# Optimization experiments

Hardware: AMD Instinct MI355X
Metric: run time of the kernel (lower is better)

The kernel has to match this reference:

```python
import jax, jax.numpy as jnp
import numpy as np

B, N, E, F, FE, H = 4, 1024, 65536, 96, 32, 12
DH = F // H
EPS = 1e-3  # keras LayerNormalization default epsilon


def layer_norm(x, g, b):
    m = jnp.mean(x, axis=-1, keepdims=True)
    v = jnp.var(x, axis=-1, keepdims=True)
    return (x - m) / jnp.sqrt(v + EPS) * g + b


def setup_inputs() -> dict:
    key = jax.random.key(0)
    ks = jax.random.split(key, 14)
    s = lambda d: 1.0 / np.sqrt(d)
    return {
        "nodes": jax.random.normal(ks[0], (B, N, F), jnp.float32),
        "edge_features": jax.random.normal(ks[1], (B, E, FE), jnp.float32),
        "distance": jax.random.uniform(ks[2], (B, E, 1), jnp.float32),
        "edges": jax.random.randint(ks[3], (B, E, 2), 0, N, jnp.int32),
        # message MLP: Dense(2F+FE -> F) + GELU + LayerNorm
        "Wm": jax.random.normal(ks[4], (2 * F + FE, F), jnp.float32) * s(2 * F + FE),
        "bm": jnp.zeros((F,), jnp.float32),
        "g1": jnp.ones((F,), jnp.float32),
        "b1": jnp.zeros((F,), jnp.float32),
        # gated multi-head self-attention over concat([nodes, aggregated]) (2F -> F)
        "Wq": jax.random.normal(ks[5], (2 * F, F), jnp.float32) * s(2 * F),
        "bq": jnp.zeros((F,), jnp.float32),
        "Wk": jax.random.normal(ks[6], (2 * F, F), jnp.float32) * s(2 * F),
        "bk": jnp.zeros((F,), jnp.float32),
        "Wv": jax.random.normal(ks[7], (2 * F, F), jnp.float32) * s(2 * F),
        "bv": jnp.zeros((F,), jnp.float32),
        "Wg": jax.random.normal(ks[8], (2 * F, F), jnp.float32) * s(2 * F),
        "bg": jnp.zeros((F,), jnp.float32),
        "Wo": jax.random.normal(ks[9], (F, F), jnp.float32) * s(F),
        "bo": jnp.zeros((F,), jnp.float32),
        "g2": jnp.ones((F,), jnp.float32),
        "b2": jnp.zeros((F,), jnp.float32),
        # learnable gaussian edge-weight params
        "sigma": jnp.full((1,), 0.005, jnp.float32),
        "beta": jnp.full((1,), 4.0, jnp.float32),
    }


def reference(nodes, edge_features, distance, edges, Wm, bm, g1, b1,
              Wq, bq, Wk, bk, Wv, bv, Wg, bg, Wo, bo, g2, b2, sigma, beta):
    # --- message: gather endpoint node features per edge ---
    gathered = jax.vmap(lambda n, e: n[e])(nodes, edges)              # [B,E,2,F]
    msg_in = jnp.concatenate([gathered.reshape(B, E, 2 * F), edge_features], axis=-1)
    messages = layer_norm(jax.nn.gelu(msg_in @ Wm + bm, approximate=False), g1, b1)  # [B,E,F]
    # --- learnable gaussian edge weighting ---
    edge_weights = jnp.exp(-((distance ** 2 / (2.0 * sigma ** 2)) ** beta))           # [B,E,1]
    weighted_messages = messages * edge_weights
    # --- scatter: per-graph segment-sum into receiver nodes (edge[:,1]) ---
    aggregated = jax.vmap(lambda m, seg: jax.ops.segment_sum(m, seg, num_segments=N))(
        weighted_messages, edges[..., 1])                             # [B,N,F]
    # --- update: gated multi-head self-attention on concat([nodes, aggregated]) ---
    x = jnp.concatenate([nodes, aggregated], axis=-1)                 # [B,N,2F]
    heads = lambda t: t.reshape(B, N, H, DH).transpose(0, 2, 1, 3)    # [B,H,N,DH]
    q, k, v = heads(x @ Wq + bq), heads(x @ Wk + bk), heads(x @ Wv + bv)
    gate = heads(jax.nn.sigmoid(x @ Wg + bg))
    attn = jax.nn.softmax(jnp.einsum("bhqd,bhkd->bhqk", q, k) / jnp.sqrt(jnp.float32(DH)), axis=-1)
    out = (jnp.einsum("bhqk,bhkd->bhqd", attn, v) * gate).transpose(0, 2, 1, 3).reshape(B, N, F)
    out = out @ Wo + bo
    updated_nodes = layer_norm(jax.nn.gelu(out, approximate=False), g2, b2)
    return (updated_nodes, weighted_messages, distance, edges)
```

## Files before the change

kernel.cpp:

```cpp
#include <hip/hip_runtime.h>
#include <math.h>

#define Bn 4
#define Nn 1024
#define En 65536
#define Fn 96
#define FEn 32
#define Hn 12

#define OUT_UPD  0
#define OUT_WM   393216LL
#define OUT_DIST 25559040LL
#define OUT_EDGE 25821184LL

#define WS_AGG  0
#define WS_Q    393216
#define WS_K    786432
#define WS_V    1179648
#define WS_G    1572864
#define WS_AO   1966080
#define WS_LIST 2359296
#define WS_LW   2424832
#define WS_CNT  2490368

#define MSG_BLOCKS 832

typedef __attribute__((ext_vector_type(8))) short bf16x8;
typedef __attribute__((ext_vector_type(4))) float f32x4;

__device__ __forceinline__ float gelu_exact(float x) {
    return 0.5f * x * (1.0f + erff(x * 0.70710678118654752f));
}

__device__ __forceinline__ unsigned cvtpk_bf16(float lo, float hi) {
    unsigned r;
    asm("v_cvt_pk_bf16_f32 %0, %1, %2" : "=v"(r) : "v"(lo), "v"(hi));
    return r;
}

__device__ __forceinline__ void zero_wm_chunk(int c, const float* __restrict__ dist,
                                              const float* __restrict__ sigma,
                                              const float* __restrict__ beta,
                                              float* __restrict__ out_wm,
                                              int tid, int nthr, int* s_act) {
    if (tid < 256) {
        int ge = c * 256 + tid;
        float d = dist[ge];
        float sg = sigma[0], bt = beta[0];
        float t = d * d / (2.0f * sg * sg);
        s_act[tid] = (powf(t, bt) < 90.0f) ? 1 : 0;
    }
    __syncthreads();
    const float4 z = make_float4(0.f, 0.f, 0.f, 0.f);
    float4* wm4 = (float4*)out_wm + (size_t)c * 6144;
    for (int p = tid; p < 6144; p += nthr) {
        if (!s_act[p / 24]) wm4[p] = z;
    }
}

__global__ void zero_kernel(float* __restrict__ agg, int* __restrict__ gcnt) {
    int i = blockIdx.x * 256 + threadIdx.x;
    const float4 z = make_float4(0.f, 0.f, 0.f, 0.f);
    float4* p = (float4*)agg;
    p[i] = z;
    p[i + 49152] = z;
    if (i == 0) gcnt[0] = 0;
}

__global__ __launch_bounds__(1024) void scan_kernel(
        const float* __restrict__ dist, const int* __restrict__ edges,
        const float* __restrict__ sigma, const float* __restrict__ beta,
        float* __restrict__ out_dist, float* __restrict__ out_edges,
        int* __restrict__ glist, float* __restrict__ gw,
        int* __restrict__ gcnt) {
    __shared__ int wcnt[16], wbase[16], blkbase;
    int tid = threadIdx.x;
    int lane = tid & 63, wv = tid >> 6;
    int ge = blockIdx.x * 1024 + tid;
    float d = dist[ge];
    out_dist[ge] = d;
    int e0 = edges[2 * ge], e1 = edges[2 * ge + 1];
    *(float2*)&out_edges[2 * ge] = make_float2((float)e0, (float)e1);
    float sg = sigma[0], bt = beta[0];
    float t  = d * d / (2.0f * sg * sg);
    float tp = powf(t, bt);
    bool active = (tp < 90.0f);
    float w = active ? expf(-tp) : 0.0f;

    unsigned long long mask = __ballot(active);
    int lp = __popcll(mask & ((1ull << lane) - 1ull));
    if (lane == 0) wcnt[wv] = __popcll(mask);
    __syncthreads();
    if (tid == 0) {
        int a = 0;
        #pragma unroll
        for (int i = 0; i < 16; ++i) { wbase[i] = a; a += wcnt[i]; }
        blkbase = a ? atomicAdd(gcnt, a) : 0;
    }
    __syncthreads();
    if (active) {
        int pos = blkbase + wbase[wv] + lp;
        if (pos < 65536) { glist[pos] = ge; gw[pos] = w; }
    }
}

__global__ __launch_bounds__(256) void msg_kernel(
        const int* __restrict__ glist, const float* __restrict__ gw,
        const int* __restrict__ gcnt, const int* __restrict__ edges,
        const float* __restrict__ nodes, const float* __restrict__ ef,
        const float* __restrict__ Wm, const float* __restrict__ bm,
        const float* __restrict__ g1, const float* __restrict__ b1,
        float* __restrict__ out_wm, float* __restrict__ agg) {
    __shared__ float sin_s[4][4][232];
    int tid = threadIdx.x;
    int lane = tid & 63, wv = tid >> 6;
    int count = gcnt[0];
    if (count > 65536) count = 65536;
    if ((int)blockIdx.x * 16 >= count) return;
    int c2 = 64 + (lane & 31);
    int wid = blockIdx.x * 4 + wv;

    for (int base = wid * 4; base < count; base += MSG_BLOCKS * 16) {
        int   gei[4];
        float wgt[4];
        bool  val[4];
        #pragma unroll
        for (int e = 0; e < 4; ++e) {
            int ai = base + e;
            val[e] = (ai < count);
            int as = val[e] ? ai : base;
            gei[e] = glist[as];
            wgt[e] = val[e] ? gw[ai] : 0.0f;
        }
        #pragma unroll
        for (int e = 0; e < 4; ++e) {
            int g = gei[e];
            int b = g >> 16;
            int e0 = edges[2 * g], e1 = edges[2 * g + 1];
            const float* n0 = nodes + ((size_t)b * Nn + e0) * 96;
            const float* n1 = nodes + ((size_t)b * Nn + e1) * 96;
            const float* ep = ef + (size_t)g * 32;
            #pragma unroll
            for (int ii = 0; ii < 4; ++ii) {
                int i = ii * 64 + lane;
                if (i < 224) {
                    float v = (i < 96) ? n0[i] : (i < 192) ? n1[i - 96] : ep[i - 192];
                    sin_s[wv][e][i] = v;
                }
            }
        }
        float acc[4][2];
        #pragma unroll
        for (int e = 0; e < 4; ++e) { acc[e][0] = bm[lane]; acc[e][1] = bm[c2]; }
        #pragma unroll 8
        for (int i = 0; i < 224; ++i) {
            float w1 = Wm[i * 96 + lane];
            float w2 = Wm[i * 96 + c2];
            #pragma unroll
            for (int e = 0; e < 4; ++e) {
                float a = sin_s[wv][e][i];
                acc[e][0] = fmaf(a, w1, acc[e][0]);
                acc[e][1] = fmaf(a, w2, acc[e][1]);
            }
        }
        #pragma unroll
        for (int e = 0; e < 4; ++e) {
            if (!val[e]) continue;
            float y1 = gelu_exact(acc[e][0]);
            float y2 = gelu_exact(acc[e][1]);
            float c2v = (lane < 32) ? y2 : 0.0f;
            float sum  = y1 + c2v;
            float sum2 = y1 * y1 + c2v * c2v;
            #pragma unroll
            for (int off = 1; off < 64; off <<= 1) {
                sum  += __shfl_xor(sum, off);
                sum2 += __shfl_xor(sum2, off);
            }
            float mean = sum * (1.0f / 96.0f);
            float var  = sum2 * (1.0f / 96.0f) - mean * mean;
            float rs   = rsqrtf(var + 1e-3f);
            int g = gei[e];
            int b = g >> 16;
            int e1 = edges[2 * g + 1];
            float* aggp = agg + ((size_t)b * Nn + e1) * 96;
            float* wmp  = out_wm + (size_t)g * 96;
            float o1 = ((y1 - mean) * rs * g1[lane] + b1[lane]) * wgt[e];
            wmp[lane] = o1;
            atomicAdd(&aggp[lane], o1);
            if (lane < 32) {
                float o2 = ((y2 - mean) * rs * g1[c2] + b1[c2]) * wgt[e];
                wmp[c2] = o2;
                atomicAdd(&aggp[c2], o2);
            }
        }
    }
}

__global__ __launch_bounds__(256, 1) void proj_kernel(
        const float* __restrict__ nodes, const float* __restrict__ agg,
        const float* __restrict__ Wq, const float* __restrict__ bq,
        const float* __restrict__ Wk, const float* __restrict__ bk,
        const float* __restrict__ Wv, const float* __restrict__ bv,
        const float* __restrict__ Wg, const float* __restrict__ bg,
        float* __restrict__ qo, float* __restrict__ ko,
        float* __restrict__ vo, float* __restrict__ go,
        const float* __restrict__ dist, const float* __restrict__ sigma,
        const float* __restrict__ beta, float* __restrict__ out_wm) {
    __shared__ float xs[192][64];
    __shared__ float Ws[192 * 96];
    __shared__ int s_act[256];
    int tid = threadIdx.x;
    int m = blockIdx.y;
    zero_wm_chunk(768 + m * 64 + blockIdx.x, dist, sigma, beta, out_wm, tid, 256, s_act);

    const float* W    = (m == 0) ? Wq : (m == 1) ? Wk : (m == 2) ? Wv : Wg;
    const float* bias = (m == 0) ? bq : (m == 1) ? bk : (m == 2) ? bv : bg;
    float* outp       = (m == 0) ? qo : (m == 1) ? ko : (m == 2) ? vo : go;
    int row0 = blockIdx.x * 64;
    int b = row0 >> 10, n0 = row0 & 1023;

    {
        float4* Ws4 = (float4*)Ws;
        const float4* Wg4 = (const float4*)W;
        for (int i = tid; i < 4608; i += 256) Ws4[i] = Wg4[i];
    }
    for (int i = tid; i < 3072; i += 256) {
        int r = i & 63, k4 = i >> 6;
        size_t row = (size_t)row0 + r;
        float4 v = (k4 < 24) ? *(const float4*)&nodes[row * 96 + k4 * 4]
                             : *(const float4*)&agg[row * 96 + (k4 - 24) * 4];
        int k = k4 * 4;
        xs[k][r] = v.x; xs[k + 1][r] = v.y; xs[k + 2][r] = v.z; xs[k + 3][r] = v.w;
    }
    __syncthreads();

    int lane = tid & 63;
    int wcol = __builtin_amdgcn_readfirstlane((tid >> 6) * 24);
    float acc[24];
    #pragma unroll
    for (int c = 0; c < 24; ++c) acc[c] = bias[wcol + c];
    for (int k = 0; k < 192; ++k) {
        float a = xs[k][lane];
        const float* wr = &Ws[k * 96 + wcol];
        #pragma unroll
        for (int c = 0; c < 24; ++c)
            acc[c] = fmaf(a, wr[c], acc[c]);
    }
    if (m == 3) {
        #pragma unroll
        for (int c = 0; c < 24; ++c) acc[c] = 1.0f / (1.0f + expf(-acc[c]));
    }
    float4* out4 = (float4*)outp;
    int h0 = wcol >> 3;
    #pragma unroll
    for (int hh = 0; hh < 3; ++hh) {
        size_t base = (((size_t)b * Hn + (h0 + hh)) * Nn + (n0 + lane)) * 2;
        out4[base]     = make_float4(acc[hh*8+0], acc[hh*8+1], acc[hh*8+2], acc[hh*8+3]);
        out4[base + 1] = make_float4(acc[hh*8+4], acc[hh*8+5], acc[hh*8+6], acc[hh*8+7]);
    }
}

__global__ __launch_bounds__(256, 4) void attn_kernel(
        const float* __restrict__ qp, const float* __restrict__ kp,
        const float* __restrict__ vp, const float* __restrict__ gp,
        float* __restrict__ ao,
        const float* __restrict__ dist, const float* __restrict__ sigma,
        const float* __restrict__ beta, float* __restrict__ out_wm) {
    __shared__ __align__(16) unsigned short K_s[1024][8];
    __shared__ __align__(16) unsigned short Vt_s[9][1032];
    __shared__ __align__(16) unsigned short P_s[4][16][32];
    __shared__ int s_act[256];
    int tid = threadIdx.x;
    zero_wm_chunk(blockIdx.y * 16 + blockIdx.x, dist, sigma, beta, out_wm, tid, 256, s_act);

    int bh = blockIdx.y;
    int lane = tid & 63, wv = tid >> 6;
    size_t hb = (size_t)bh * (Nn * 8);
    const float* kc = kp + hb;
    const float* vc = vp + hb;

    {
        const float2* k2 = (const float2*)kc;
        unsigned* kw = (unsigned*)&K_s[0][0];
        for (int i = tid; i < 4096; i += 256) {
            float2 v = k2[i];
            kw[i] = cvtpk_bf16(v.x, v.y);
        }
    }
    {
        const float4* v4 = (const float4*)vc;
        for (int i = tid; i < 1024; i += 256) {
            int kp2 = i >> 1, dq = i & 1;
            float4 a = v4[kp2 * 4 + dq];
            float4 b = v4[kp2 * 4 + 2 + dq];
            int d0 = dq * 4;
            ((unsigned*)&Vt_s[d0 + 0][0])[kp2] = cvtpk_bf16(a.x, b.x);
            ((unsigned*)&Vt_s[d0 + 1][0])[kp2] = cvtpk_bf16(a.y, b.y);
            ((unsigned*)&Vt_s[d0 + 2][0])[kp2] = cvtpk_bf16(a.z, b.z);
            ((unsigned*)&Vt_s[d0 + 3][0])[kp2] = cvtpk_bf16(a.w, b.w);
        }
        unsigned* ow = (unsigned*)&Vt_s[8][0];
        for (int i = tid; i < 516; i += 256) ow[i] = 0x3F803F80u;
    }
    const float scale = 0.35355339059327376f;
    int qbase = blockIdx.x * 64 + wv * 16;
    bf16x8 aq = {0, 0, 0, 0, 0, 0, 0, 0};
    if (lane < 16) {
        const float* qr = qp + hb + (size_t)(qbase + lane) * 8;
        float4 qa = *(const float4*)qr;
        float4 qb2 = *(const float4*)(qr + 4);
        union { unsigned u[4]; bf16x8 v; } U;
        U.u[0] = cvtpk_bf16(qa.x * scale, qa.y * scale);
        U.u[1] = cvtpk_bf16(qa.z * scale, qa.w * scale);
        U.u[2] = cvtpk_bf16(qb2.x * scale, qb2.y * scale);
        U.u[3] = cvtpk_bf16(qb2.z * scale, qb2.w * scale);
        aq = U.v;
    }
    __syncthreads();

    const bf16x8 zero8 = {0, 0, 0, 0, 0, 0, 0, 0};
    const f32x4 zero4 = {0.f, 0.f, 0.f, 0.f};
    f32x4 o = zero4;
    int n16 = lane & 15, grp = lane >> 4;
    for (int c = 0; c < 32; ++c) {
        bf16x8 bk0 = zero8, bk1 = zero8;
        if (lane < 16) {
            bk0 = *(const bf16x8*)&K_s[c * 32 + lane][0];
            bk1 = *(const bf16x8*)&K_s[c * 32 + 16 + lane][0];
        }
        f32x4 s0 = __builtin_amdgcn_mfma_f32_16x16x32_bf16(aq, bk0, zero4, 0, 0, 0);
        f32x4 s1 = __builtin_amdgcn_mfma_f32_16x16x32_bf16(aq, bk1, zero4, 0, 0, 0);
        #pragma unroll
        for (int r = 0; r < 4; ++r) {
            unsigned pk = cvtpk_bf16(__expf(s0[r]), __expf(s1[r]));
            int row = grp * 4 + r;
            P_s[wv][row][n16]      = (unsigned short)pk;
            P_s[wv][row][16 + n16] = (unsigned short)(pk >> 16);
        }
        bf16x8 pa = *(const bf16x8*)&P_s[wv][n16][grp * 8];
        bf16x8 bv = zero8;
        if (n16 <= 8) bv = *(const bf16x8*)&Vt_s[n16][c * 32 + grp * 8];
        o = __builtin_amdgcn_mfma_f32_16x16x32_bf16(pa, bv, o, 0, 0, 0);
    }

    #pragma unroll
    for (int r = 0; r < 4; ++r) {
        float L = __shfl(o[r], (lane & 48) | 8);
        if (n16 < 8) {
            int q = qbase + grp * 4 + r;
            size_t off = hb + (size_t)q * 8 + n16;
            ao[off] = o[r] / L * gp[off];
        }
    }
}

__global__ __launch_bounds__(256) void out_kernel(
        const float* __restrict__ ao, const float* __restrict__ Wo,
        const float* __restrict__ bo, const float* __restrict__ g2,
        const float* __restrict__ b2, float* __restrict__ out0) {
    __shared__ float as_[96][64];
    __shared__ float Ws[96 * 96];
    __shared__ float2 red_s[4][64];
    int tid = threadIdx.x;
    int row0 = blockIdx.x * 64;
    int b = row0 >> 10, n0 = row0 & 1023;
    {
        float4* W4 = (float4*)Ws;
        const float4* Wg4 = (const float4*)Wo;
        for (int i = tid; i < 2304; i += 256) W4[i] = Wg4[i];
    }
    const float2* ao2 = (const float2*)ao;
    for (int i = tid; i < 3072; i += 256) {
        int n = i & 63, hd = i >> 6;
        int h = hd >> 2, dp = hd & 3;
        float2 v = ao2[(((size_t)b * Hn + h) * Nn + (n0 + n)) * 4 + dp];
        as_[h * 8 + dp * 2][n]     = v.x;
        as_[h * 8 + dp * 2 + 1][n] = v.y;
    }
    __syncthreads();
    int lane = tid & 63, w = tid >> 6;
    int wcol = __builtin_amdgcn_readfirstlane(w * 24);
    float acc[24];
    #pragma unroll
    for (int c = 0; c < 24; ++c) acc[c] = bo[wcol + c];
    for (int k = 0; k < 96; ++k) {
        float a = as_[k][lane];
        const float* wr = &Ws[k * 96 + wcol];
        #pragma unroll
        for (int c = 0; c < 24; ++c)
            acc[c] = fmaf(a, wr[c], acc[c]);
    }
    float y[24];
    float sum = 0.0f, sum2 = 0.0f;
    #pragma unroll
    for (int c = 0; c < 24; ++c) {
        float g = gelu_exact(acc[c]);
        y[c] = g; sum += g; sum2 += g * g;
    }
    red_s[w][lane] = make_float2(sum, sum2);
    __syncthreads();
    float S = 0.0f, S2 = 0.0f;
    #pragma unroll
    for (int i = 0; i < 4; ++i) { float2 p = red_s[i][lane]; S += p.x; S2 += p.y; }
    float mean = S * (1.0f / 96.0f);
    float var  = S2 * (1.0f / 96.0f) - mean * mean;
    float rs   = rsqrtf(var + 1e-3f);
    size_t row = (size_t)row0 + lane;
    #pragma unroll
    for (int c = 0; c < 24; ++c)
        y[c] = (y[c] - mean) * rs * g2[wcol + c] + b2[wcol + c];
    float4* o4 = (float4*)&out0[row * 96 + wcol];
    #pragma unroll
    for (int q = 0; q < 6; ++q)
        o4[q] = make_float4(y[q*4], y[q*4+1], y[q*4+2], y[q*4+3]);
}

extern "C" void kernel_launch(void* const* d_in, const int* in_sizes, int n_in,
                              void* d_out, int out_size, void* d_ws, size_t ws_size,
                              hipStream_t stream) {
    const float* nodes = (const float*)d_in[0];
    const float* ef    = (const float*)d_in[1];
    const float* dist  = (const float*)d_in[2];
    const int*   edges = (const int*)d_in[3];
    const float* Wm = (const float*)d_in[4];
    const float* bm = (const float*)d_in[5];
    const float* g1 = (const float*)d_in[6];
    const float* b1 = (const float*)d_in[7];
    const float* Wq = (const float*)d_in[8];
    const float* bq = (const float*)d_in[9];
    const float* Wk = (const float*)d_in[10];
    const float* bk = (const float*)d_in[11];
    const float* Wv = (const float*)d_in[12];
    const float* bv = (const float*)d_in[13];
    const float* Wg = (const float*)d_in[14];
    const float* bg = (const float*)d_in[15];
    const float* Wo = (const float*)d_in[16];
    const float* bo = (const float*)d_in[17];
    const float* g2 = (const float*)d_in[18];
    const float* b2 = (const float*)d_in[19];
    const float* sigma = (const float*)d_in[20];
    const float* beta  = (const float*)d_in[21];

    float* out = (float*)d_out;
    float* ws  = (float*)d_ws;

    float* agg  = ws + WS_AGG;
    float* qb   = ws + WS_Q;
    float* kb   = ws + WS_K;
    float* vb   = ws + WS_V;
    float* gwb  = ws + WS_G;
    float* aob  = ws + WS_AO;
    int*   glist = (int*)(ws + WS_LIST);
    float* glw   = ws + WS_LW;
    int*   gcnt  = (int*)(ws + WS_CNT);

    zero_kernel<<<192, 256, 0, stream>>>(agg, gcnt);

    scan_kernel<<<Bn * En / 1024, 1024, 0, stream>>>(
        dist, edges, sigma, beta, out + OUT_DIST, out + OUT_EDGE, glist, glw, gcnt);

    msg_kernel<<<MSG_BLOCKS, 256, 0, stream>>>(
        glist, glw, gcnt, edges, nodes, ef, Wm, bm, g1, b1, out + OUT_WM, agg);

    dim3 gp_(64, 4);
    proj_kernel<<<gp_, 256, 0, stream>>>(
        nodes, agg, Wq, bq, Wk, bk, Wv, bv, Wg, bg, qb, kb, vb, gwb,
        dist, sigma, beta, out + OUT_WM);

    dim3 ga(16, Bn * Hn);
    attn_kernel<<<ga, 256, 0, stream>>>(qb, kb, vb, gwb, aob,
                                        dist, sigma, beta, out + OUT_WM);

    out_kernel<<<Bn * Nn / 64, 256, 0, stream>>>(aob, Wo, bo, g2, b2, out + OUT_UPD);
}
```

Measured before the change: 110.2 us.

## Fuse edge scan and message computation into one per-block kernel

Combines the global active-edge compaction and the message MLP into a single kernel where each 256-edge block compacts its active edges in shared memory and processes them locally. This drops the global atomic counter, the global list buffers, a separate zero kernel and a launch. The zeroing of inactive weighted-message rows moves out of the projection and attention kernels into the fused kernel. The trade-off is possible load imbalance, since work per block now depends on how many active edges it holds, and the agg buffer is cleared with a memset.

After: 103.1 us. -6.5%, faster.

```diff
diff --git a/kernel.cpp b/kernel.cpp
--- a/kernel.cpp
+++ b/kernel.cpp
@@ -19,11 +19,6 @@
 #define WS_V    1179648
 #define WS_G    1572864
 #define WS_AO   1966080
-#define WS_LIST 2359296
-#define WS_LW   2424832
-#define WS_CNT  2490368
-
-#define MSG_BLOCKS 832
 
 typedef __attribute__((ext_vector_type(8))) short bf16x8;
 typedef __attribute__((ext_vector_type(4))) float f32x4;
@@ -38,99 +33,72 @@
     return r;
 }
 
-__device__ __forceinline__ void zero_wm_chunk(int c, const float* __restrict__ dist,
-                                              const float* __restrict__ sigma,
-                                              const float* __restrict__ beta,
-                                              float* __restrict__ out_wm,
-                                              int tid, int nthr, int* s_act) {
-    if (tid < 256) {
-        int ge = c * 256 + tid;
-        float d = dist[ge];
-        float sg = sigma[0], bt = beta[0];
-        float t = d * d / (2.0f * sg * sg);
-        s_act[tid] = (powf(t, bt) < 90.0f) ? 1 : 0;
-    }
-    __syncthreads();
-    const float4 z = make_float4(0.f, 0.f, 0.f, 0.f);
-    float4* wm4 = (float4*)out_wm + (size_t)c * 6144;
-    for (int p = tid; p < 6144; p += nthr) {
-        if (!s_act[p / 24]) wm4[p] = z;
-    }
-}
-
-__global__ void zero_kernel(float* __restrict__ agg, int* __restrict__ gcnt) {
-    int i = blockIdx.x * 256 + threadIdx.x;
-    const float4 z = make_float4(0.f, 0.f, 0.f, 0.f);
-    float4* p = (float4*)agg;
-    p[i] = z;
-    p[i + 49152] = z;
-    if (i == 0) gcnt[0] = 0;
-}
-
-__global__ __launch_bounds__(1024) void scan_kernel(
+__global__ __launch_bounds__(256) void scanmsg_kernel(
         const float* __restrict__ dist, const int* __restrict__ edges,
         const float* __restrict__ sigma, const float* __restrict__ beta,
+        const float* __restrict__ nodes, const float* __restrict__ ef,
+        const float* __restrict__ Wm, const float* __restrict__ bm,
+        const float* __restrict__ g1, const float* __restrict__ b1,
         float* __restrict__ out_dist, float* __restrict__ out_edges,
-        int* __restrict__ glist, float* __restrict__ gw,
-        int* __restrict__ gcnt) {
-    __shared__ int wcnt[16], wbase[16], blkbase;
+        float* __restrict__ out_wm, float* __restrict__ agg) {
+    __shared__ int   s_ge[256];
+    __shared__ float s_w[256];
+    __shared__ int   s_act[256];
+    __shared__ int   wcnt[4], wbase[4];
+    __shared__ float sin_s[4][4][232];
     int tid = threadIdx.x;
-    int lane = tid & 63, wv = tid >> 6;
-    int ge = blockIdx.x * 1024 + tid;
+    int blk = blockIdx.x;
+    int ge = blk * 256 + tid;
+
     float d = dist[ge];
     out_dist[ge] = d;
-    int e0 = edges[2 * ge], e1 = edges[2 * ge + 1];
-    *(float2*)&out_edges[2 * ge] = make_float2((float)e0, (float)e1);
+    int e0s = edges[2 * ge], e1s = edges[2 * ge + 1];
+    *(float2*)&out_edges[2 * ge] = make_float2((float)e0s, (float)e1s);
     float sg = sigma[0], bt = beta[0];
     float t  = d * d / (2.0f * sg * sg);
     float tp = powf(t, bt);
     bool active = (tp < 90.0f);
     float w = active ? expf(-tp) : 0.0f;
+    s_act[tid] = active ? 1 : 0;
 
     unsigned long long mask = __ballot(active);
+    int lane = tid & 63, wv = tid >> 6;
     int lp = __popcll(mask & ((1ull << lane) - 1ull));
     if (lane == 0) wcnt[wv] = __popcll(mask);
     __syncthreads();
     if (tid == 0) {
         int a = 0;
         #pragma unroll
-        for (int i = 0; i < 16; ++i) { wbase[i] = a; a += wcnt[i]; }
-        blkbase = a ? atomicAdd(gcnt, a) : 0;
+        for (int i = 0; i < 4; ++i) { wbase[i] = a; a += wcnt[i]; }
     }
     __syncthreads();
     if (active) {
-        int pos = blkbase + wbase[wv] + lp;
-        if (pos < 65536) { glist[pos] = ge; gw[pos] = w; }
-    }
-}
-
-__global__ __launch_bounds__(256) void msg_kernel(
-        const int* __restrict__ glist, const float* __restrict__ gw,
-        const int* __restrict__ gcnt, const int* __restrict__ edges,
-        const float* __restrict__ nodes, const float* __restrict__ ef,
-        const float* __restrict__ Wm, const float* __restrict__ bm,
-        const float* __restrict__ g1, const float* __restrict__ b1,
-        float* __restrict__ out_wm, float* __restrict__ agg) {
-    __shared__ float sin_s[4][4][232];
-    int tid = threadIdx.x;
-    int lane = tid & 63, wv = tid >> 6;
-    int count = gcnt[0];
-    if (count > 65536) count = 65536;
-    if ((int)blockIdx.x * 16 >= count) return;
+        int pos = wbase[wv] + lp;
+        s_ge[pos] = ge;
+        s_w[pos]  = w;
+    }
+    __syncthreads();
+    int count = wbase[3] + wcnt[3];
+
+    {
+        const float4 z = make_float4(0.f, 0.f, 0.f, 0.f);
+        float4* wm4 = (float4*)out_wm + (size_t)blk * 6144;
+        for (int p = tid; p < 6144; p += 256) {
+            if (!s_act[p / 24]) wm4[p] = z;
+        }
+    }
+
     int c2 = 64 + (lane & 31);
-    int wid = blockIdx.x * 4 + wv;
-
-    for (int base = wid * 4; base < count; base += MSG_BLOCKS * 16) {
+    for (int qb = wv * 4; qb < count; qb += 16) {
         int   gei[4];
         float wgt[4];
         bool  val[4];
         #pragma unroll
         for (int e = 0; e < 4; ++e) {
-            int ai = base + e;
+            int ai = qb + e;
             val[e] = (ai < count);
-            int as = val[e] ? ai : base;
-            gei[e] = glist[as];
-            wgt[e] = val[e] ? gw[ai] : 0.0f;
+            gei[e] = s_ge[val[e] ? ai : qb];
+            wgt[e] = val[e] ? s_w[ai] : 0.0f;
         }
         #pragma unroll
         for (int e = 0; e < 4; ++e) {
@@ -203,16 +171,11 @@
         const float* __restrict__ Wv, const float* __restrict__ bv,
         const float* __restrict__ Wg, const float* __restrict__ bg,
         float* __restrict__ qo, float* __restrict__ ko,
-        float* __restrict__ vo, float* __restrict__ go,
-        const float* __restrict__ dist, const float* __restrict__ sigma,
-        const float* __restrict__ beta, float* __restrict__ out_wm) {
+        float* __restrict__ vo, float* __restrict__ go) {
     __shared__ float xs[192][64];
     __shared__ float Ws[192 * 96];
-    __shared__ int s_act[256];
     int tid = threadIdx.x;
     int m = blockIdx.y;
-    zero_wm_chunk(768 + m * 64 + blockIdx.x, dist, sigma, beta, out_wm, tid, 256, s_act);
-
     const float* W    = (m == 0) ? Wq : (m == 1) ? Wk : (m == 2) ? Wv : Wg;
     const float* bias = (m == 0) ? bq : (m == 1) ? bk : (m == 2) ? bv : bg;
     float* outp       = (m == 0) ? qo : (m == 1) ? ko : (m == 2) ? vo : go;
@@ -263,16 +226,11 @@
 __global__ __launch_bounds__(256, 4) void attn_kernel(
         const float* __restrict__ qp, const float* __restrict__ kp,
         const float* __restrict__ vp, const float* __restrict__ gp,
-        float* __restrict__ ao,
-        const float* __restrict__ dist, const float* __restrict__ sigma,
-        const float* __restrict__ beta, float* __restrict__ out_wm) {
+        float* __restrict__ ao) {
     __shared__ __align__(16) unsigned short K_s[1024][8];
     __shared__ __align__(16) unsigned short Vt_s[9][1032];
     __shared__ __align__(16) unsigned short P_s[4][16][32];
-    __shared__ int s_act[256];
     int tid = threadIdx.x;
-    zero_wm_chunk(blockIdx.y * 16 + blockIdx.x, dist, sigma, beta, out_wm, tid, 256, s_act);
-
     int bh = blockIdx.y;
     int lane = tid & 63, wv = tid >> 6;
     size_t hb = (size_t)bh * (Nn * 8);
@@ -450,26 +408,19 @@
     float* vb   = ws + WS_V;
     float* gwb  = ws + WS_G;
     float* aob  = ws + WS_AO;
-    int*   glist = (int*)(ws + WS_LIST);
-    float* glw   = ws + WS_LW;
-    int*   gcnt  = (int*)(ws + WS_CNT);
-
-    zero_kernel<<<192, 256, 0, stream>>>(agg, gcnt);
-
-    scan_kernel<<<Bn * En / 1024, 1024, 0, stream>>>(
-        dist, edges, sigma, beta, out + OUT_DIST, out + OUT_EDGE, glist, glw, gcnt);
-
-    msg_kernel<<<MSG_BLOCKS, 256, 0, stream>>>(
-        glist, glw, gcnt, edges, nodes, ef, Wm, bm, g1, b1, out + OUT_WM, agg);
+
+    hipMemsetAsync(agg, 0, (size_t)Bn * Nn * Fn * sizeof(float), stream);
+
+    scanmsg_kernel<<<Bn * En / 256, 256, 0, stream>>>(
+        dist, edges, sigma, beta, nodes, ef, Wm, bm, g1, b1,
+        out + OUT_DIST, out + OUT_EDGE, out + OUT_WM, agg);
 
     dim3 gp_(64, 4);
     proj_kernel<<<gp_, 256, 0, stream>>>(
-        nodes, agg, Wq, bq, Wk, bk, Wv, bv, Wg, bg, qb, kb, vb, gwb,
-        dist, sigma, beta, out + OUT_WM);
+        nodes, agg, Wq, bq, Wk, bk, Wv, bv, Wg, bg, qb, kb, vb, gwb);
 
     dim3 ga(16, Bn * Hn);
-    attn_kernel<<<ga, 256, 0, stream>>>(qb, kb, vb, gwb, aob,
-                                        dist, sigma, beta, out + OUT_WM);
+    attn_kernel<<<ga, 256, 0, stream>>>(qb, kb, vb, gwb, aob);
 
     out_kernel<<<Bn * Nn / 64, 256, 0, stream>>>(aob, Wo, bo, g2, b2, out + OUT_UPD);
 }
```
